# Kernel tuning notes

Hardware: AMD Instinct MI355X
Metric: run time of the kernel (lower is better)

## Reference

```python
import jax, jax.numpy as jnp
import numpy as np

T = 16          # time_span
N = 128         # num_trajectory
D = 512         # embedding dim
TEMP = 0.1      # temperature
INF = 1000000000.0
M = 2 * N * T   # total rows of z (two views)


def setup_inputs() -> dict:
    key = jax.random.key(0)
    k1, k2 = jax.random.split(key)
    z = jax.random.normal(k1, (M, D), dtype=jnp.float32)
    done = jax.random.randint(k2, (T, N), 0, 2).astype(jnp.int32)  # [T, N] binary done flags
    return {"z": z, "done": done}


def _build_positive_mask(done):
    # done: [T, N] int -> transposed to [N, T] as in the torch code
    d = done.astype(jnp.float32).T  # [N, T]
    # Sequential rewrite loop is equivalent to:
    #   done_new[r,t] = 1 iff exists original done at p < t in row r AND orig done[r,t] == 0
    excl = jnp.cumsum(d, axis=1) - d  # exclusive cumsum along time
    d_new = jnp.where((excl > 0) & (d == 0), 1.0, 0.0)  # [N, T]
    done_vec = 1.0 - d_new.reshape(-1)  # [N*T]
    # block-diagonal temporal mask: same trajectory => 1
    traj = jnp.arange(N * T) // T
    block = (traj[:, None] == traj[None, :]).astype(jnp.float32)  # [NT, NT]
    done_mask = (done_vec[:, None] * done_vec[None, :]) * block
    done_mask = jnp.tile(done_mask, (2, 2))      # [M, M]
    temporal_mask = jnp.tile(block, (2, 2))      # [M, M]
    eye = jnp.eye(M, dtype=jnp.float32)
    positive_mask = (1.0 - done_mask) * (1.0 - temporal_mask) + eye
    return positive_mask, eye


def reference(z, done):
    positive_mask, eye = _build_positive_mask(done)
    # cosine similarity = normalize + GEMM (same math as broadcasted F.cosine_similarity)
    norms = jnp.maximum(jnp.linalg.norm(z, axis=-1, keepdims=True), 1e-8)
    zn = z / norms
    logits = (zn @ zn.T) / TEMP - eye * INF  # [M, M]
    log_probs = jax.nn.log_softmax(logits, axis=1)
    neg = 1.0 - positive_mask
    mean_log_prob = jnp.sum(neg * log_probs, axis=1) / jnp.sum(neg, axis=1)
    return -jnp.mean(mean_log_prob)
```

## Files before the change

### kernel.cpp

```cpp
#include <hip/hip_runtime.h>
#include <hip/hip_bf16.h>

typedef __bf16 bf16x8 __attribute__((ext_vector_type(8)));
typedef float f32x16 __attribute__((ext_vector_type(16)));
typedef unsigned int u32x4 __attribute__((ext_vector_type(4)));
typedef unsigned short u16;


__global__ void nrm_kernel(const float* __restrict__ z, u16* __restrict__ zn,
                           float* __restrict__ expsum, float* __restrict__ possum) {
    int row = blockIdx.x;
    int tid = threadIdx.x;
    float4 v = ((const float4*)(z + row * 512))[tid];
    float ss = v.x * v.x + v.y * v.y + v.z * v.z + v.w * v.w;
#pragma unroll
    for (int off = 32; off; off >>= 1) ss += __shfl_down(ss, off, 64);
    __shared__ float red[2];
    if ((tid & 63) == 0) red[tid >> 6] = ss;
    __syncthreads();
    float norm = fmaxf(sqrtf(red[0] + red[1]), 1e-8f);
    float sc = 1.0f / norm;
    __hip_bfloat16 b[4];
    b[0] = __float2bfloat16(v.x * sc);
    b[1] = __float2bfloat16(v.y * sc);
    b[2] = __float2bfloat16(v.z * sc);
    b[3] = __float2bfloat16(v.w * sc);
    uint2 p;
    __builtin_memcpy(&p, b, 8);
    ((uint2*)(zn + row * 512))[tid] = p;
    if (tid == 0) { expsum[row] = 0.f; possum[row] = 0.f; }
}

__global__ __launch_bounds__(256, 2) void gemm_kernel(const u16* __restrict__ zn,
                                                      float* __restrict__ expsum,
                                                      float* __restrict__ possum) {
    if (blockIdx.x >= 528) {
        if (threadIdx.x < 64) {
            int g = blockIdx.x - 528;
            int l = threadIdx.x;
            int u = l & 31, h2 = l >> 5;
            int grow = (u < 16) ? (g * 16 + u) : (2048 + g * 16 + (u - 16));
            const u32x4* src = (const u32x4*)(zn + grow * 512);
            f32x16 acc = {};
#pragma unroll
            for (int kc = 0; kc < 32; ++kc) {
                bf16x8 f = __builtin_bit_cast(bf16x8, src[h2 + 2 * kc]);
                acc = __builtin_amdgcn_mfma_f32_32x32x16_bf16(f, f, acc, 0, 0, 0);
            }
#pragma unroll
            for (int r = 0; r < 16; ++r) {
                int rrow = (r & 3) + 8 * (r >> 2) + 4 * h2;
                float v = (rrow == u) ? 0.f : acc[r];
                v += __shfl_xor(v, 1, 64);
                v += __shfl_xor(v, 2, 64);
                v += __shfl_xor(v, 4, 64);
                v += __shfl_xor(v, 8, 64);
                v += __shfl_xor(v, 16, 64);
                if (u == 0) {
                    int gr = (rrow < 16) ? (g * 16 + rrow) : (2048 + g * 16 + (rrow - 16));
                    possum[gr] = v * 10.0f;
                }
            }
        }
        return;
    }

    __shared__ u16 Bt[2][32 * 512];

    int b = blockIdx.x;
    int ti = 0;
    while (b >= 32 - ti) { b -= 32 - ti; ++ti; }
    int tj = ti + b;

    int wave = threadIdx.x >> 6;
    int l = threadIdx.x & 63;
    int m = l & 31, h = l >> 5;
    int rowbase = ti * 128 + wave * 32;
    int colbase = tj * 128;
    bool diag = (ti == tj);

    u32x4 a[32];
    const u32x4* arow = (const u32x4*)(zn + (rowbase + m) * 512);
#pragma unroll
    for (int kc = 0; kc < 32; ++kc) a[kc] = arow[h + 2 * kc];

    float racc[16];
#pragma unroll
    for (int r = 0; r < 16; ++r) racc[r] = 0.f;

    int c = threadIdx.x >> 3;
    int g0 = threadIdx.x & 7;
    int woff = c * 64 + (g0 ^ (c & 7));
    const u16* zsrc = zn + (colbase + c) * 512;

    u32x4 stg[8];
    {
        const u32x4* src = (const u32x4*)zsrc;
#pragma unroll
        for (int i = 0; i < 8; ++i) stg[i] = src[g0 + 8 * i];
        u32x4* dst = ((u32x4*)Bt[0]) + woff;
#pragma unroll
        for (int i = 0; i < 8; ++i) dst[8 * i] = stg[i];
    }

    int sw0 = m & 1, sw12 = (m >> 1) & 3;
    int rbyte[4];
#pragma unroll
    for (int q = 0; q < 4; ++q)
        rbyte[q] = m * 1024 + (h ^ sw0) * 16 + ((q ^ sw12) * 32);

    const char* rb = (const char*)Bt[0];
    char* wb = (char*)Bt[1];
    __syncthreads();

    for (int ct = 0; ct < 4; ++ct) {
        if (ct < 3) {
            const u32x4* src = (const u32x4*)(zsrc + (ct + 1) * 32 * 512);
#pragma unroll
            for (int i = 0; i < 8; ++i) stg[i] = src[g0 + 8 * i];
        }
        f32x16 acc = {};
        __builtin_amdgcn_s_setprio(1);
#pragma unroll
        for (int kg = 0; kg < 8; ++kg) {
#pragma unroll
            for (int q = 0; q < 4; ++q) {
                bf16x8 bf = *(const bf16x8*)(rb + rbyte[q] + kg * 128);
                acc = __builtin_amdgcn_mfma_f32_32x32x16_bf16(
                    __builtin_bit_cast(bf16x8, a[4 * kg + q]), bf, acc, 0, 0, 0);
            }
        }
        __builtin_amdgcn_s_setprio(0);

        if (diag && ct == wave) {
#pragma unroll
            for (int r = 0; r < 16; ++r) {
                int rrow = (r & 3) + 8 * (r >> 2) + 4 * h;
                if (rrow != m) racc[r] += __builtin_exp2f(acc[r] * 14.426950408889634f);
            }
        } else {
            float csum = 0.f;
#pragma unroll
            for (int r = 0; r < 16; ++r) {
                float e = __builtin_exp2f(acc[r] * 14.426950408889634f);
                racc[r] += e;
                csum += e;
            }
            if (!diag) {
                csum += __shfl_xor(csum, 32, 64);
                if (h == 0) atomicAdd(&expsum[colbase + ct * 32 + m], csum);
            }
        }

        if (ct < 3) {
            u32x4* dst = ((u32x4*)wb) + woff;
#pragma unroll
            for (int i = 0; i < 8; ++i) dst[8 * i] = stg[i];
        }
        __syncthreads();
        const char* t = rb; rb = (const char*)wb; wb = (char*)t;
    }

#pragma unroll
    for (int r = 0; r < 16; ++r) {
        float v = racc[r];
        v += __shfl_xor(v, 1, 64);
        v += __shfl_xor(v, 2, 64);
        v += __shfl_xor(v, 4, 64);
        v += __shfl_xor(v, 8, 64);
        v += __shfl_xor(v, 16, 64);
        if (m == 0) {
            int rrow = (r & 3) + 8 * (r >> 2) + 4 * h;
            atomicAdd(&expsum[rowbase + rrow], v);
        }
    }
}

__global__ void fin_kernel(const float* __restrict__ expsum,
                           const float* __restrict__ possum, float* __restrict__ out) {
    int tid = threadIdx.x;
    float s = 0.f;
    for (int i = tid; i < 4096; i += 1024)
        s += __logf(expsum[i]) - possum[i] * (1.0f / 31.0f);
#pragma unroll
    for (int off = 32; off; off >>= 1) s += __shfl_down(s, off, 64);
    __shared__ float red[16];
    if ((tid & 63) == 0) red[tid >> 6] = s;
    __syncthreads();
    if (tid == 0) {
        float t = 0.f;
#pragma unroll
        for (int i = 0; i < 16; ++i) t += red[i];
        out[0] = t * (1.0f / 4096.0f);
    }
}

extern "C" void kernel_launch(void* const* d_in, const int* in_sizes, int n_in,
                              void* d_out, int out_size, void* d_ws, size_t ws_size,
                              hipStream_t stream) {
    const float* z = (const float*)d_in[0];
    u16* zn = (u16*)d_ws;
    float* expsum = (float*)((char*)d_ws + (4u << 20));
    float* possum = expsum + 4096;
    float* out = (float*)d_out;

    nrm_kernel<<<4096, 128, 0, stream>>>(z, zn, expsum, possum);
    gemm_kernel<<<656, 256, 0, stream>>>(zn, expsum, possum);
    fin_kernel<<<1, 1024, 0, stream>>>(expsum, possum, out);
}
```

Before: 95.56 us.

## Stage B tiles via direct global-to-LDS loads and use one wave per row in normalize

```diff
diff --git a/kernel.cpp b/kernel.cpp
--- a/kernel.cpp
+++ b/kernel.cpp
@@ -8,55 +8,63 @@
 
 
 __global__ void nrm_kernel(const float* __restrict__ z, u16* __restrict__ zn,
-                           float* __restrict__ expsum, float* __restrict__ possum) {
-    int row = blockIdx.x;
+                           float* __restrict__ expsum) {
     int tid = threadIdx.x;
-    float4 v = ((const float4*)(z + row * 512))[tid];
-    float ss = v.x * v.x + v.y * v.y + v.z * v.z + v.w * v.w;
-#pragma unroll
-    for (int off = 32; off; off >>= 1) ss += __shfl_down(ss, off, 64);
-    __shared__ float red[2];
-    if ((tid & 63) == 0) red[tid >> 6] = ss;
-    __syncthreads();
-    float norm = fmaxf(sqrtf(red[0] + red[1]), 1e-8f);
-    float sc = 1.0f / norm;
-    __hip_bfloat16 b[4];
-    b[0] = __float2bfloat16(v.x * sc);
-    b[1] = __float2bfloat16(v.y * sc);
-    b[2] = __float2bfloat16(v.z * sc);
-    b[3] = __float2bfloat16(v.w * sc);
-    uint2 p;
-    __builtin_memcpy(&p, b, 8);
-    ((uint2*)(zn + row * 512))[tid] = p;
-    if (tid == 0) { expsum[row] = 0.f; possum[row] = 0.f; }
+    int l = tid & 63, w = tid >> 6;
+    int row = blockIdx.x * 4 + w;
+    const float4* src = (const float4*)(z + row * 512);
+    float4 v0 = src[l];
+    float4 v1 = src[l + 64];
+    float ss = v0.x * v0.x + v0.y * v0.y + v0.z * v0.z + v0.w * v0.w
+             + v1.x * v1.x + v1.y * v1.y + v1.z * v1.z + v1.w * v1.w;
+#pragma unroll
+    for (int off = 32; off; off >>= 1) ss += __shfl_xor(ss, off, 64);
+    float sc = 1.0f / fmaxf(sqrtf(ss), 1e-8f);
+    __hip_bfloat16 b0[4], b1[4];
+    b0[0] = __float2bfloat16(v0.x * sc); b0[1] = __float2bfloat16(v0.y * sc);
+    b0[2] = __float2bfloat16(v0.z * sc); b0[3] = __float2bfloat16(v0.w * sc);
+    b1[0] = __float2bfloat16(v1.x * sc); b1[1] = __float2bfloat16(v1.y * sc);
+    b1[2] = __float2bfloat16(v1.z * sc); b1[3] = __float2bfloat16(v1.w * sc);
+    uint2 p0, p1;
+    __builtin_memcpy(&p0, b0, 8);
+    __builtin_memcpy(&p1, b1, 8);
+    ((uint2*)(zn + row * 512))[l] = p0;
+    ((uint2*)(zn + row * 512))[l + 64] = p1;
+    int gi = blockIdx.x * 256 + tid;
+    if (gi < 4096) expsum[gi] = 0.f;
 }
 
 __global__ __launch_bounds__(256, 2) void gemm_kernel(const u16* __restrict__ zn,
                                                       float* __restrict__ expsum,
                                                       float* __restrict__ possum) {
+    __shared__ u16 Bt[2][32 * 512];
+
+    int tid = threadIdx.x;
+    int wave = tid >> 6;
+    int l = tid & 63;
+    int m = l & 31, h = l >> 5;
+
     if (blockIdx.x >= 528) {
-        if (threadIdx.x < 64) {
+        if (tid < 64) {
             int g = blockIdx.x - 528;
-            int l = threadIdx.x;
-            int u = l & 31, h2 = l >> 5;
-            int grow = (u < 16) ? (g * 16 + u) : (2048 + g * 16 + (u - 16));
+            int grow = (m < 16) ? (g * 16 + m) : (2048 + g * 16 + (m - 16));
             const u32x4* src = (const u32x4*)(zn + grow * 512);
             f32x16 acc = {};
 #pragma unroll
             for (int kc = 0; kc < 32; ++kc) {
-                bf16x8 f = __builtin_bit_cast(bf16x8, src[h2 + 2 * kc]);
+                bf16x8 f = __builtin_bit_cast(bf16x8, src[h + 2 * kc]);
                 acc = __builtin_amdgcn_mfma_f32_32x32x16_bf16(f, f, acc, 0, 0, 0);
             }
 #pragma unroll
             for (int r = 0; r < 16; ++r) {
-                int rrow = (r & 3) + 8 * (r >> 2) + 4 * h2;
-                float v = (rrow == u) ? 0.f : acc[r];
+                int rrow = (r & 3) + 8 * (r >> 2) + 4 * h;
+                float v = (rrow == m) ? 0.f : acc[r];
                 v += __shfl_xor(v, 1, 64);
                 v += __shfl_xor(v, 2, 64);
                 v += __shfl_xor(v, 4, 64);
                 v += __shfl_xor(v, 8, 64);
                 v += __shfl_xor(v, 16, 64);
-                if (u == 0) {
+                if (m == 0) {
                     int gr = (rrow < 16) ? (g * 16 + rrow) : (2048 + g * 16 + (rrow - 16));
                     possum[gr] = v * 10.0f;
                 }
@@ -64,17 +72,12 @@
         }
         return;
     }
-
-    __shared__ u16 Bt[2][32 * 512];
 
     int b = blockIdx.x;
     int ti = 0;
     while (b >= 32 - ti) { b -= 32 - ti; ++ti; }
     int tj = ti + b;
 
-    int wave = threadIdx.x >> 6;
-    int l = threadIdx.x & 63;
-    int m = l & 31, h = l >> 5;
     int rowbase = ti * 128 + wave * 32;
     int colbase = tj * 128;
     bool diag = (ti == tj);
@@ -88,37 +91,32 @@
 #pragma unroll
     for (int r = 0; r < 16; ++r) racc[r] = 0.f;
 
-    int c = threadIdx.x >> 3;
-    int g0 = threadIdx.x & 7;
-    int woff = c * 64 + (g0 ^ (c & 7));
-    const u16* zsrc = zn + (colbase + c) * 512;
-
-    u32x4 stg[8];
-    {
-        const u32x4* src = (const u32x4*)zsrc;
-#pragma unroll
-        for (int i = 0; i < 8; ++i) stg[i] = src[g0 + 8 * i];
-        u32x4* dst = ((u32x4*)Bt[0]) + woff;
-#pragma unroll
-        for (int i = 0; i < 8; ++i) dst[8 * i] = stg[i];
-    }
-
     int sw0 = m & 1, sw12 = (m >> 1) & 3;
     int rbyte[4];
 #pragma unroll
     for (int q = 0; q < 4; ++q)
         rbyte[q] = m * 1024 + (h ^ sw0) * 16 + ((q ^ sw12) * 32);
 
-    const char* rb = (const char*)Bt[0];
-    char* wb = (char*)Bt[1];
+#define STAGE(bufidx, cb)                                                          \
+    {                                                                              \
+        u16* buf_ = (u16*)Bt[bufidx];                                              \
+        _Pragma("unroll")                                                          \
+        for (int i_ = 0; i_ < 8; ++i_) {                                           \
+            int cc_ = wave * 8 + i_;                                               \
+            const u16* gsrc_ = zn + ((cb) + cc_) * 512 + ((l ^ (cc_ & 7)) * 8);    \
+            __builtin_amdgcn_global_load_lds(                                      \
+                (const __attribute__((address_space(1))) unsigned int*)gsrc_,      \
+                (__attribute__((address_space(3))) unsigned int*)(buf_ + cc_ * 512), \
+                16, 0, 0);                                                         \
+        }                                                                          \
+    }
+
+    STAGE(0, colbase)
     __syncthreads();
 
     for (int ct = 0; ct < 4; ++ct) {
-        if (ct < 3) {
-            const u32x4* src = (const u32x4*)(zsrc + (ct + 1) * 32 * 512);
-#pragma unroll
-            for (int i = 0; i < 8; ++i) stg[i] = src[g0 + 8 * i];
-        }
+        if (ct < 3) STAGE((ct + 1) & 1, colbase + (ct + 1) * 32)
+        const char* rb = (const char*)Bt[ct & 1];
         f32x16 acc = {};
         __builtin_amdgcn_s_setprio(1);
 #pragma unroll
@@ -151,14 +149,7 @@
                 if (h == 0) atomicAdd(&expsum[colbase + ct * 32 + m], csum);
             }
         }
-
-        if (ct < 3) {
-            u32x4* dst = ((u32x4*)wb) + woff;
-#pragma unroll
-            for (int i = 0; i < 8; ++i) dst[8 * i] = stg[i];
-        }
         __syncthreads();
-        const char* t = rb; rb = (const char*)wb; wb = (char*)t;
     }
 
 #pragma unroll
@@ -204,7 +195,7 @@
     float* possum = expsum + 4096;
     float* out = (float*)d_out;
 
-    nrm_kernel<<<4096, 128, 0, stream>>>(z, zn, expsum, possum);
+    nrm_kernel<<<1024, 256, 0, stream>>>(z, zn, expsum);
     gemm_kernel<<<656, 256, 0, stream>>>(zn, expsum, possum);
     fin_kernel<<<1, 1024, 0, stream>>>(expsum, possum, out);
 }
```

Measured after the change: 109.0 us. 14.0% more time.
